# Kernel tuning notes

Hardware: AMD Instinct MI355X
Metric: run time of the kernel (lower is better)

Reference implementation:

```python
import jax, jax.numpy as jnp
import numpy as np

ATT_DIM = 1024
N_HEADS = 16
D_HEAD = ATT_DIM // N_HEADS
LARGE = 1e30  # fp32 masking constant used by masked_softmax


def setup_inputs() -> dict:
    key = jax.random.key(0)
    ks = jax.random.split(key, 12)
    B, Tq, Tv, D = 4, 2048, 2048, 1024
    s = 1.0 / np.sqrt(D)
    sf = 1.0 / np.sqrt(ATT_DIM)
    return {
        "query": jax.random.normal(ks[0], (B, Tq, D), jnp.float32),
        "value": jax.random.normal(ks[1], (B, Tv, D), jnp.float32),
        "value_lens": jax.random.randint(ks[2], (B,), 0, Tv, jnp.int32),
        "Wq": jax.random.normal(ks[3], (D, ATT_DIM), jnp.float32) * s,
        "bq": jnp.zeros((ATT_DIM,), jnp.float32),
        "Wk": jax.random.normal(ks[4], (D, ATT_DIM), jnp.float32) * s,
        "bk": jnp.zeros((ATT_DIM,), jnp.float32),
        "Wv": jax.random.normal(ks[5], (D, ATT_DIM), jnp.float32) * s,
        "bv": jnp.zeros((ATT_DIM,), jnp.float32),
        "Wf": jax.random.normal(ks[6], (ATT_DIM, ATT_DIM), jnp.float32) * sf,
        "bf": jnp.zeros((ATT_DIM,), jnp.float32),
    }


def _attention(query, value, value_lens, Wq, bq, Wk, bk, Wv, bv, Wf, bf):
    B, Tq, _ = query.shape
    Tv = value.shape[1]
    # projections
    k = value @ Wk + bk                     # [B,Tv,att_dim]
    v = value @ Wv + bv                     # [B,Tv,att_dim]
    q = (query @ Wq + bq) / jnp.sqrt(jnp.asarray(D_HEAD, query.dtype))
    # split heads
    q = q.reshape(B, Tq, N_HEADS, D_HEAD)
    k = k.reshape(B, Tv, N_HEADS, D_HEAD)
    v = v.reshape(B, Tv, N_HEADS, D_HEAD)
    # energy: [B, n_heads, Tq, Tv]
    energy = jnp.einsum("bind,bjnd->bnij", q, k)
    # sequence mask: [B,1,1,Tv]
    mask = (jnp.arange(Tv)[None, :] < value_lens[:, None]).astype(energy.dtype)
    energy = energy - (1.0 - mask)[:, None, None, :] * jnp.asarray(LARGE, energy.dtype)
    att_weight = jax.nn.softmax(energy, axis=-1)
    # context: [B, Tq, n_heads, d_head] -> [B, Tq, att_dim]
    context = jnp.einsum("bnij,bjnd->bind", att_weight, v).reshape(B, Tq, ATT_DIM)
    return context @ Wf + bf  # final_att (num_att_head > 1)


def reference(query, value, value_lens, Wq, bq, Wk, bk, Wv, bv, Wf, bf):
    return _attention(query, value, value_lens, Wq, bq, Wk, bk, Wv, bv, Wf, bf)
```

## Files before the change

### kernel.cpp

```cpp
#include <hip/hip_runtime.h>
#include <hip/hip_bf16.h>

typedef __attribute__((ext_vector_type(8))) short short8;
typedef __attribute__((ext_vector_type(4))) float f32x4;
typedef unsigned short u16;
typedef unsigned int u32;
typedef __attribute__((ext_vector_type(8))) unsigned short u16x8;
typedef __attribute__((ext_vector_type(4))) unsigned short u16x4;

__device__ __forceinline__ u16 f2bf(float f) {
    u32 u = __builtin_bit_cast(u32, f);
    u += 0x7FFFu + ((u >> 16) & 1u);
    return (u16)(u >> 16);
}
__device__ __forceinline__ u32 cvtpk(float a, float b) {
    u32 r;
    asm("v_cvt_pk_bf16_f32 %0, %1, %2" : "=v"(r) : "v"(a), "v"(b));
    return r;
}
__device__ __forceinline__ float fexp2(float x) {
    float r;
    asm("v_exp_f32 %0, %1" : "=v"(r) : "v"(x));
    return r;
}

__device__ __forceinline__ int swz(int row, int col) {
    return (row * 128 + col * 2) ^ ((row & 7) << 4);
}

__device__ __forceinline__ void gl16(const void* g, void* l) {
    __builtin_amdgcn_global_load_lds(
        (const __attribute__((address_space(1))) unsigned int*)g,
        (__attribute__((address_space(3))) unsigned int*)l, 16, 0, 0);
}

#define FENCE() asm volatile("" ::: "memory")
#define BARRIER() do { FENCE(); __builtin_amdgcn_s_barrier(); FENCE(); } while (0)

__global__ __launch_bounds__(256)
void prep_kernel(const float* __restrict__ query, const float* __restrict__ value,
                 u16* __restrict__ qB, u16* __restrict__ vB,
                 const float* __restrict__ W0, const float* __restrict__ W1,
                 const float* __restrict__ W2, const float* __restrict__ W3,
                 u16* __restrict__ T0, u16* __restrict__ T1,
                 u16* __restrict__ T2, u16* __restrict__ T3)
{
    int bid = blockIdx.x;
    if (bid < 8192) {
        const float* src; u16* dst;
        if (bid < 4096) { src = query; dst = qB; }
        else            { src = value; dst = vB; bid -= 4096; }
        const int i = bid * 256 + threadIdx.x;
        const float4 a = ((const float4*)src)[2 * i];
        const float4 b = ((const float4*)src)[2 * i + 1];
        u16x8 h;
        h[0] = f2bf(a.x); h[1] = f2bf(a.y); h[2] = f2bf(a.z); h[3] = f2bf(a.w);
        h[4] = f2bf(b.x); h[5] = f2bf(b.y); h[6] = f2bf(b.z); h[7] = f2bf(b.w);
        ((u16x8*)dst)[i] = h;
        return;
    }
    int b2 = bid - 8192;
    const int z = b2 >> 10; b2 &= 1023;
    const float* W; u16* T;
    switch (z) {
        case 0:  W = W0; T = T0; break;
        case 1:  W = W1; T = T1; break;
        case 2:  W = W2; T = T2; break;
        default: W = W3; T = T3; break;
    }
    __shared__ u16 tile[32][33];
    const int tid = threadIdx.x;
    const int n0 = (b2 & 31) * 32, k0 = (b2 >> 5) * 32;
    const int r = tid >> 3, c = (tid & 7) * 4;
    float4 v = *(const float4*)(W + (size_t)(k0 + r) * 1024 + n0 + c);
    tile[c + 0][r] = f2bf(v.x);
    tile[c + 1][r] = f2bf(v.y);
    tile[c + 2][r] = f2bf(v.z);
    tile[c + 3][r] = f2bf(v.w);
    __syncthreads();
    u16x4 h;
    h[0] = tile[r][c]; h[1] = tile[r][c + 1]; h[2] = tile[r][c + 2]; h[3] = tile[r][c + 3];
    *(u16x4*)(T + (size_t)(n0 + r) * 1024 + k0 + c) = h;
}

#define GNK 32

__device__ __forceinline__ void stage_a(const u16* __restrict__ A, unsigned char* bufA,
                                        int row0, int kt, int tid) {
    const int r = tid >> 2, s = tid & 3;
    gl16((const unsigned char*)A + (size_t)(row0 + r) * 2048 + kt * 64 + ((s ^ (r & 3)) << 4),
         bufA + tid * 16);
}
__device__ __forceinline__ void stage_b(const u16* __restrict__ BT, unsigned char* bufB,
                                        int col0, int kt, int hb, int tid) {
    const int r = hb * 128 + (tid >> 2), s = tid & 3;
    gl16((const unsigned char*)BT + (size_t)(col0 + r) * 2048 + kt * 64 + ((s ^ (r & 3)) << 4),
         bufB + hb * 8192 + tid * 16);
}

__device__ __forceinline__ void gemm_core(const u16* __restrict__ A, const u16* __restrict__ BT,
                                          int row0, int col0, unsigned char* smem,
                                          int tid, int wm, int wn, int l15, int lhi,
                                          f32x4 acc[4][4])
{
    const int slot = (lhi ^ (l15 & 3)) << 4;
    #pragma unroll
    for (int kt = 0; kt < 2; ++kt) {
        unsigned char* buf = smem + kt * 24576;
        stage_a(A, buf, row0, kt, tid);
        stage_b(BT, buf + 8192, col0, kt, 0, tid);
        stage_b(BT, buf + 8192, col0, kt, 1, tid);
    }
    asm volatile("s_waitcnt vmcnt(3)" ::: "memory");
    BARRIER();

    int cb = 0;
    for (int k = 0; k < GNK; ++k) {
        unsigned char* bufA = smem + cb * 24576;
        unsigned char* bufB = bufA + 8192;
        const bool st = (k + 2 < GNK);
        int nb = cb + 2; if (nb >= 3) nb -= 3;
        unsigned char* nbuf = smem + nb * 24576;
        cb = (cb == 2) ? 0 : cb + 1;

        short8 a0, a1, a2, a3, b0, b1;
        a0 = *(const short8*)(bufA + (wm * 64 + 0 * 16 + l15) * 64 + slot);
        a1 = *(const short8*)(bufA + (wm * 64 + 1 * 16 + l15) * 64 + slot);
        a2 = *(const short8*)(bufA + (wm * 64 + 2 * 16 + l15) * 64 + slot);
        a3 = *(const short8*)(bufA + (wm * 64 + 3 * 16 + l15) * 64 + slot);
        b0 = *(const short8*)(bufB + (wn * 64 + 0 * 16 + l15) * 64 + slot);
        b1 = *(const short8*)(bufB + (wn * 64 + 1 * 16 + l15) * 64 + slot);
        if (st) stage_a(A, nbuf, row0, k + 2, tid);
        BARRIER();
        __builtin_amdgcn_s_setprio(1);
        acc[0][0] = __builtin_amdgcn_mfma_f32_16x16x32_bf16(a0, b0, acc[0][0], 0, 0, 0);
        acc[0][1] = __builtin_amdgcn_mfma_f32_16x16x32_bf16(a0, b1, acc[0][1], 0, 0, 0);
        acc[1][0] = __builtin_amdgcn_mfma_f32_16x16x32_bf16(a1, b0, acc[1][0], 0, 0, 0);
        acc[1][1] = __builtin_amdgcn_mfma_f32_16x16x32_bf16(a1, b1, acc[1][1], 0, 0, 0);
        acc[2][0] = __builtin_amdgcn_mfma_f32_16x16x32_bf16(a2, b0, acc[2][0], 0, 0, 0);
        acc[2][1] = __builtin_amdgcn_mfma_f32_16x16x32_bf16(a2, b1, acc[2][1], 0, 0, 0);
        acc[3][0] = __builtin_amdgcn_mfma_f32_16x16x32_bf16(a3, b0, acc[3][0], 0, 0, 0);
        acc[3][1] = __builtin_amdgcn_mfma_f32_16x16x32_bf16(a3, b1, acc[3][1], 0, 0, 0);
        __builtin_amdgcn_s_setprio(0);
        BARRIER();

        short8 b2, b3;
        b2 = *(const short8*)(bufB + (wn * 64 + 2 * 16 + l15) * 64 + slot);
        b3 = *(const short8*)(bufB + (wn * 64 + 3 * 16 + l15) * 64 + slot);
        if (st) {
            stage_b(BT, nbuf + 8192, col0, k + 2, 0, tid);
            stage_b(BT, nbuf + 8192, col0, k + 2, 1, tid);
        }
        if (k < GNK - 2)       asm volatile("s_waitcnt vmcnt(3)" ::: "memory");
        else if (k == GNK - 2) asm volatile("s_waitcnt vmcnt(0)" ::: "memory");
        BARRIER();
        __builtin_amdgcn_s_setprio(1);
        acc[0][2] = __builtin_amdgcn_mfma_f32_16x16x32_bf16(a0, b2, acc[0][2], 0, 0, 0);
        acc[0][3] = __builtin_amdgcn_mfma_f32_16x16x32_bf16(a0, b3, acc[0][3], 0, 0, 0);
        acc[1][2] = __builtin_amdgcn_mfma_f32_16x16x32_bf16(a1, b2, acc[1][2], 0, 0, 0);
        acc[1][3] = __builtin_amdgcn_mfma_f32_16x16x32_bf16(a1, b3, acc[1][3], 0, 0, 0);
        acc[2][2] = __builtin_amdgcn_mfma_f32_16x16x32_bf16(a2, b2, acc[2][2], 0, 0, 0);
        acc[2][3] = __builtin_amdgcn_mfma_f32_16x16x32_bf16(a2, b3, acc[2][3], 0, 0, 0);
        acc[3][2] = __builtin_amdgcn_mfma_f32_16x16x32_bf16(a3, b2, acc[3][2], 0, 0, 0);
        acc[3][3] = __builtin_amdgcn_mfma_f32_16x16x32_bf16(a3, b3, acc[3][3], 0, 0, 0);
        __builtin_amdgcn_s_setprio(0);
        BARRIER();
    }
}

__global__ __launch_bounds__(512, 4)
void proj_kernel(const u16* __restrict__ queryB, const u16* __restrict__ valueB,
                 const u16* __restrict__ WqT, const u16* __restrict__ WkT,
                 const u16* __restrict__ WvT,
                 const float* __restrict__ bq, const float* __restrict__ bk,
                 const float* __restrict__ bv,
                 u16* __restrict__ Qb, u16* __restrict__ Kb, u16* __restrict__ Vt)
{
    __shared__ __align__(16) unsigned char smem[73728];
    const int t = (blockIdx.x & 7) * 96 + (blockIdx.x >> 3);
    const int z = t >> 8;
    const int tile = t & 255;
    const int row0 = (tile >> 2) * 128, col0 = (tile & 3) * 256;

    const u16* A    = (z == 0) ? queryB : valueB;
    const u16* BT   = (z == 0) ? WqT : (z == 1) ? WkT : WvT;
    const float* bias = (z == 0) ? bq : (z == 1) ? bk : bv;

    const int tid = threadIdx.x;
    const int lane = tid & 63, w = tid >> 6;
    const int wm = w >> 2, wn = w & 3;
    const int l15 = lane & 15, lhi = lane >> 4;

    f32x4 acc[4][4];
    const f32x4 fz = {0.f, 0.f, 0.f, 0.f};
    #pragma unroll
    for (int m = 0; m < 4; ++m)
        #pragma unroll
        for (int n = 0; n < 4; ++n) acc[m][n] = fz;

    gemm_core(A, BT, row0, col0, smem, tid, wm, wn, l15, lhi, acc);

    if (z < 2) {
        u16* out = (z == 0) ? Qb : Kb;
        const float scale = (z == 0) ? 0.18033688011112042f : 1.0f;
        const int bb = row0 >> 11;
        #pragma unroll
        for (int n = 0; n < 4; ++n) {
            int col = col0 + wn * 64 + n * 16 + l15;
            int hh = col >> 6, d = col & 63;
            float bv2 = bias[col];
            #pragma unroll
            for (int m = 0; m < 4; ++m) {
                int rbase = row0 + wm * 64 + m * 16 + lhi * 4;
                #pragma unroll
                for (int rr = 0; rr < 4; ++rr) {
                    int trow = (rbase + rr) & 2047;
                    out[(((size_t)bb * 16 + hh) * 2048 + trow) * 64 + d] =
                        f2bf((acc[m][n][rr] + bv2) * scale);
                }
            }
        }
    } else {
        __syncthreads();
        u16* vl = (u16*)smem;
        #pragma unroll
        for (int n = 0; n < 4; ++n) {
            int c = wn * 64 + n * 16 + l15;
            float bv2 = bias[col0 + c];
            #pragma unroll
            for (int m = 0; m < 4; ++m) {
                int rl = wm * 64 + m * 16 + lhi * 4;
                u16x4 h;
                #pragma unroll
                for (int rr = 0; rr < 4; ++rr) h[rr] = f2bf(acc[m][n][rr] + bv2);
                *(u16x4*)(vl + c * 132 + rl) = h;
            }
        }
        __syncthreads();
        const int bb = row0 >> 11, t0 = row0 & 2047;
        const int c = tid >> 1, hseg = tid & 1;
        const int col = col0 + c;
        const int hh = col >> 6, d = col & 63;
        size_t gb = (((size_t)bb * 16 + hh) * 64 + d) * 2048 + t0 + hseg * 64;
        #pragma unroll
        for (int j = 0; j < 8; ++j) {
            u16x8 v = *(const u16x8*)(vl + c * 132 + hseg * 64 + j * 8);
            *(u16x8*)(Vt + gb + j * 8) = v;
        }
    }
}

__global__ __launch_bounds__(512, 4)
void fgemm_kernel(const u16* __restrict__ Ctx, const u16* __restrict__ WfT,
                  const float* __restrict__ bias, float* __restrict__ out)
{
    __shared__ __align__(16) unsigned char smem[73728];
    const int t = (blockIdx.x & 7) * 32 + (blockIdx.x >> 3);
    const int row0 = (t >> 2) * 128, col0 = (t & 3) * 256;

    const int tid = threadIdx.x;
    const int lane = tid & 63, w = tid >> 6;
    const int wm = w >> 2, wn = w & 3;
    const int l15 = lane & 15, lhi = lane >> 4;

    f32x4 acc[4][4];
    const f32x4 fz = {0.f, 0.f, 0.f, 0.f};
    #pragma unroll
    for (int m = 0; m < 4; ++m)
        #pragma unroll
        for (int n = 0; n < 4; ++n) acc[m][n] = fz;

    gemm_core(Ctx, WfT, row0, col0, smem, tid, wm, wn, l15, lhi, acc);

    #pragma unroll
    for (int n = 0; n < 4; ++n) {
        int col = col0 + wn * 64 + n * 16 + l15;
        float bv2 = bias[col];
        #pragma unroll
        for (int m = 0; m < 4; ++m) {
            int rbase = row0 + wm * 64 + m * 16 + lhi * 4;
            #pragma unroll
            for (int rr = 0; rr < 4; ++rr)
                out[(size_t)(rbase + rr) * 1024 + col] = acc[m][n][rr] + bv2;
        }
    }
}

__global__ __launch_bounds__(512, 4)
void attn_kernel(const u16* __restrict__ Qb, const u16* __restrict__ Kb,
                 const u16* __restrict__ Vt, const int* __restrict__ lens,
                 u16* __restrict__ Ctx)
{
    __shared__ __align__(16) unsigned char ksm[2][8192];
    __shared__ __align__(16) unsigned char vsm[2][8192];

    const int tid = threadIdx.x;
    const int lane = tid & 63;
    const int w = tid >> 6;
    const int l15 = lane & 15, lhi = lane >> 4;
    const int u = blockIdx.x;
    const int b = (u >> 8) & 3;
    const int v = u & 255;
    const int qt = (v >> 3) & 15;
    const int hh = ((v >> 7) & 1) * 8 + (v & 7);
    const size_t head = (size_t)(b * 16 + hh);
    const unsigned char* Kbase = (const unsigned char*)Kb + head * (2048 * 128);
    const unsigned char* Vbase = (const unsigned char*)Vt + head * (2048 * 128);
    const unsigned char* Qbase = (const unsigned char*)Qb + head * (2048 * 128) + (size_t)qt * (128 * 128);

    const int o0 = w * 1024 + lane * 16;
    const int r0 = o0 >> 7;
    const int sc0 = (o0 & 127) ^ ((r0 & 7) << 4);

    const unsigned char* kp = Kbase + (size_t)r0 * 128 + sc0;
    const unsigned char* vp = Vbase + (size_t)r0 * 4096 + sc0;

    const int lens_b = lens[b];
    const bool uniform = (lens_b == 0);
    const int len = uniform ? 2048 : lens_b;
    const int nt = (len + 63) >> 6;
    const bool tail = (!uniform) && ((len & 63) != 0);

    auto stage = [&](int t, int bi) {
        gl16(kp + (size_t)t * 8192, ksm[bi] + o0);
        gl16(vp + (size_t)t * 128, vsm[bi] + o0);
    };
    stage(0, 0);

    short8 qa[2];
    #pragma unroll
    for (int ks = 0; ks < 2; ++ks)
        qa[ks] = *(const short8*)(Qbase + (w * 16 + l15) * 128 + ks * 64 + lhi * 16);

    short8 onesv;
    #pragma unroll
    for (int i = 0; i < 8; ++i) onesv[i] = (short)0x3F80;

    __syncthreads();

    float m = -1e30f;
    const f32x4 fz = {0.f, 0.f, 0.f, 0.f};
    f32x4 cs = fz;
    f32x4 cT[4];
    #pragma unroll
    for (int nf = 0; nf < 4; ++nf) cT[nf] = fz;

    const int srcA = l15 + (((2 * lhi) & 3) << 4);
    const int srcB = l15 + (((2 * lhi + 1) & 3) << 4);
    const bool hi = lhi >= 2;

    for (int t = 0; t < nt; ++t) {
        const int cur = t & 1;
        if (t + 1 < nt) stage(t + 1, cur ^ 1);

        f32x4 s[4];
        #pragma unroll
        for (int jf = 0; jf < 4; ++jf) s[jf] = fz;
        if (!uniform) {
            __builtin_amdgcn_s_setprio(1);
            #pragma unroll
            for (int ks = 0; ks < 2; ++ks)
                #pragma unroll
                for (int jf = 0; jf < 4; ++jf) {
                    short8 kb = *(const short8*)(ksm[cur] + swz(jf * 16 + l15, ks * 32 + lhi * 8));
                    s[jf] = __builtin_amdgcn_mfma_f32_16x16x32_bf16(kb, qa[ks], s[jf], 0, 0, 0);
                }
            __builtin_amdgcn_s_setprio(0);
            if (tail && t == nt - 1) {
                const int kvb = t * 64 + lhi * 4;
                #pragma unroll
                for (int jf = 0; jf < 4; ++jf)
                    #pragma unroll
                    for (int r = 0; r < 4; ++r)
                        if (kvb + jf * 16 + r >= len) s[jf][r] = -1e30f;
            }
        }
        f32x4 m4;
        #pragma unroll
        for (int r = 0; r < 4; ++r)
            m4[r] = fmaxf(fmaxf(s[0][r], s[1][r]), fmaxf(s[2][r], s[3][r]));
        float tmax = fmaxf(fmaxf(m4[0], m4[1]), fmaxf(m4[2], m4[3]));
        tmax = fmaxf(tmax, __shfl_xor(tmax, 16));
        tmax = fmaxf(tmax, __shfl_xor(tmax, 32));
        if (__any(tmax > m + 8.f)) {
            const float mnew = fmaxf(m, tmax);
            const float sc = fexp2(m - mnew);
            #pragma unroll
            for (int r = 0; r < 4; ++r) cs[r] *= sc;
            #pragma unroll
            for (int nf = 0; nf < 4; ++nf)
                #pragma unroll
                for (int r = 0; r < 4; ++r) cT[nf][r] *= sc;
            m = mnew;
        }
        #pragma unroll
        for (int jf = 0; jf < 4; ++jf)
            #pragma unroll
            for (int r = 0; r < 4; ++r)
                s[jf][r] = fexp2(s[jf][r] - m);
        u32 pk[4][2];
        #pragma unroll
        for (int jf = 0; jf < 4; ++jf) {
            pk[jf][0] = cvtpk(s[jf][0], s[jf][1]);
            pk[jf][1] = cvtpk(s[jf][2], s[jf][3]);
        }
        short8 pb[2];
        #pragma unroll
        for (int ks = 0; ks < 2; ++ks) {
            u32 a0, a1, a2, a3;
            { u32 x0 = (u32)__shfl((int)pk[2 * ks][0], srcA); u32 x1 = (u32)__shfl((int)pk[2 * ks + 1][0], srcA); a0 = hi ? x1 : x0; }
            { u32 x0 = (u32)__shfl((int)pk[2 * ks][1], srcA); u32 x1 = (u32)__shfl((int)pk[2 * ks + 1][1], srcA); a1 = hi ? x1 : x0; }
            { u32 x0 = (u32)__shfl((int)pk[2 * ks][0], srcB); u32 x1 = (u32)__shfl((int)pk[2 * ks + 1][0], srcB); a2 = hi ? x1 : x0; }
            { u32 x0 = (u32)__shfl((int)pk[2 * ks][1], srcB); u32 x1 = (u32)__shfl((int)pk[2 * ks + 1][1], srcB); a3 = hi ? x1 : x0; }
            typedef __attribute__((ext_vector_type(4))) unsigned int u32x4_t;
            u32x4_t av = {a0, a1, a2, a3};
            pb[ks] = __builtin_bit_cast(short8, av);
        }
        __builtin_amdgcn_s_setprio(1);
        #pragma unroll
        for (int ks = 0; ks < 2; ++ks) {
            cs = __builtin_amdgcn_mfma_f32_16x16x32_bf16(onesv, pb[ks], cs, 0, 0, 0);
            #pragma unroll
            for (int nf = 0; nf < 4; ++nf) {
                short8 vb = *(const short8*)(vsm[cur] + swz(nf * 16 + l15, ks * 32 + lhi * 8));
                cT[nf] = __builtin_amdgcn_mfma_f32_16x16x32_bf16(vb, pb[ks], cT[nf], 0, 0, 0);
            }
        }
        __builtin_amdgcn_s_setprio(0);
        __syncthreads();
    }

    const float inv = 1.0f / cs[0];
    const int trow = qt * 128 + w * 16 + l15;
    u16* op = Ctx + ((size_t)b * 2048 + trow) * 1024 + hh * 64 + lhi * 4;
    #pragma unroll
    for (int nf = 0; nf < 4; ++nf) {
        u16x4 h;
        #pragma unroll
        for (int r = 0; r < 4; ++r) h[r] = f2bf(cT[nf][r] * inv);
        *(u16x4*)(op + nf * 16) = h;
    }
}

extern "C" void kernel_launch(void* const* d_in, const int* in_sizes, int n_in,
                              void* d_out, int out_size, void* d_ws, size_t ws_size,
                              hipStream_t stream)
{
    (void)in_sizes; (void)n_in; (void)out_size; (void)ws_size;
    const float* query = (const float*)d_in[0];
    const float* value = (const float*)d_in[1];
    const int*   lens  = (const int*)d_in[2];
    const float* Wq = (const float*)d_in[3];
    const float* bq = (const float*)d_in[4];
    const float* Wk = (const float*)d_in[5];
    const float* bk = (const float*)d_in[6];
    const float* Wv = (const float*)d_in[7];
    const float* bv = (const float*)d_in[8];
    const float* Wf = (const float*)d_in[9];
    const float* bfp = (const float*)d_in[10];

    unsigned char* ws = (unsigned char*)d_ws;
    const size_t MB = (size_t)1 << 20;
    u16* WqT = (u16*)(ws + 0 * MB);
    u16* WkT = (u16*)(ws + 2 * MB);
    u16* WvT = (u16*)(ws + 4 * MB);
    u16* WfT = (u16*)(ws + 6 * MB);
    u16* Qb  = (u16*)(ws + 8 * MB);
    u16* Kb  = (u16*)(ws + 24 * MB);
    u16* Vt  = (u16*)(ws + 40 * MB);
    u16* Ctx = (u16*)(ws + 56 * MB);

    u16* queryB = (u16*)d_out;
    u16* valueB = queryB + (size_t)8192 * 1024;

    prep_kernel<<<dim3(12288), dim3(256), 0, stream>>>(query, value, queryB, valueB,
                                                       Wq, Wk, Wv, Wf, WqT, WkT, WvT, WfT);

    proj_kernel<<<dim3(768), dim3(512), 0, stream>>>(queryB, valueB, WqT, WkT, WvT,
                                                     bq, bk, bv, Qb, Kb, Vt);

    attn_kernel<<<dim3(1024), dim3(512), 0, stream>>>(Qb, Kb, Vt, lens, Ctx);

    fgemm_kernel<<<dim3(256), dim3(512), 0, stream>>>(Ctx, WfT, bfp, (float*)d_out);
}
```

Measured before the change: 173.9 us.

## Split KV range across two wave groups per block and loop batches inside block

Restructures the attention kernel so each 512-thread block handles 64 query rows for one head, with two groups of four waves each processing half of every 128-key tile. The two partial softmax states are merged through shared memory at the end. Each block now loops over all four batches, and the grid shrinks from 1024 to 512 blocks. The aim is better load balance across the variable value_lens and larger KV tiles per barrier, at the cost of 64KB of LDS (lower occupancy), an extra merge step, and serialised batch processing within a block.

Result: slower. 190.6 us (+9.7%).

```diff
diff --git a/kernel.cpp b/kernel.cpp
--- a/kernel.cpp
+++ b/kernel.cpp
@@ -26,6 +26,9 @@
 
 __device__ __forceinline__ int swz(int row, int col) {
     return (row * 128 + col * 2) ^ ((row & 7) << 4);
+}
+__device__ __forceinline__ int swzV(int row, int col) {
+    return (row * 256 + col * 2) ^ ((row & 7) << 4);
 }
 
 __device__ __forceinline__ void gl16(const void* g, void* l) {
@@ -291,154 +294,185 @@
                  const u16* __restrict__ Vt, const int* __restrict__ lens,
                  u16* __restrict__ Ctx)
 {
-    __shared__ __align__(16) unsigned char ksm[2][8192];
-    __shared__ __align__(16) unsigned char vsm[2][8192];
+    __shared__ __align__(16) unsigned char sm[65536];
+    float* mb1 = (float*)(sm + 16384);
+    float* mb2 = (float*)(sm + 49152);
 
     const int tid = threadIdx.x;
     const int lane = tid & 63;
     const int w = tid >> 6;
+    const int g = w >> 2;
+    const int wq = w & 3;
     const int l15 = lane & 15, lhi = lane >> 4;
+
     const int u = blockIdx.x;
-    const int b = (u >> 8) & 3;
-    const int v = u & 255;
-    const int qt = (v >> 3) & 15;
-    const int hh = ((v >> 7) & 1) * 8 + (v & 7);
-    const size_t head = (size_t)(b * 16 + hh);
-    const unsigned char* Kbase = (const unsigned char*)Kb + head * (2048 * 128);
-    const unsigned char* Vbase = (const unsigned char*)Vt + head * (2048 * 128);
-    const unsigned char* Qbase = (const unsigned char*)Qb + head * (2048 * 128) + (size_t)qt * (128 * 128);
-
-    const int o0 = w * 1024 + lane * 16;
-    const int r0 = o0 >> 7;
-    const int sc0 = (o0 & 127) ^ ((r0 & 7) << 4);
-
-    const unsigned char* kp = Kbase + (size_t)r0 * 128 + sc0;
-    const unsigned char* vp = Vbase + (size_t)r0 * 4096 + sc0;
-
-    const int lens_b = lens[b];
-    const bool uniform = (lens_b == 0);
-    const int len = uniform ? 2048 : lens_b;
-    const int nt = (len + 63) >> 6;
-    const bool tail = (!uniform) && ((len & 63) != 0);
-
-    auto stage = [&](int t, int bi) {
-        gl16(kp + (size_t)t * 8192, ksm[bi] + o0);
-        gl16(vp + (size_t)t * 128, vsm[bi] + o0);
-    };
-    stage(0, 0);
-
-    short8 qa[2];
-    #pragma unroll
-    for (int ks = 0; ks < 2; ++ks)
-        qa[ks] = *(const short8*)(Qbase + (w * 16 + l15) * 128 + ks * 64 + lhi * 16);
+    const int hh = ((u >> 3) & 1) * 8 + (u & 7);
+    const int qt = u >> 4;
+
+    const int o0 = tid * 16;
+    const int r0k = o0 >> 7;
+    const int sck = (o0 & 127) ^ ((r0k & 7) << 4);
+    const int r0v = o0 >> 8;
+    const int scv = (o0 & 255) ^ ((r0v & 7) << 4);
 
     short8 onesv;
     #pragma unroll
     for (int i = 0; i < 8; ++i) onesv[i] = (short)0x3F80;
 
-    __syncthreads();
-
-    float m = -1e30f;
-    const f32x4 fz = {0.f, 0.f, 0.f, 0.f};
-    f32x4 cs = fz;
-    f32x4 cT[4];
-    #pragma unroll
-    for (int nf = 0; nf < 4; ++nf) cT[nf] = fz;
-
     const int srcA = l15 + (((2 * lhi) & 3) << 4);
     const int srcB = l15 + (((2 * lhi + 1) & 3) << 4);
     const bool hi = lhi >= 2;
-
-    for (int t = 0; t < nt; ++t) {
-        const int cur = t & 1;
-        if (t + 1 < nt) stage(t + 1, cur ^ 1);
-
-        f32x4 s[4];
-        #pragma unroll
-        for (int jf = 0; jf < 4; ++jf) s[jf] = fz;
-        if (!uniform) {
+    const f32x4 fz = {0.f, 0.f, 0.f, 0.f};
+
+    for (int b = 0; b < 4; ++b) {
+        const size_t head = (size_t)(b * 16 + hh);
+        const unsigned char* Kp = (const unsigned char*)Kb + head * 262144 + r0k * 128 + sck;
+        const unsigned char* Vp = (const unsigned char*)Vt + head * 262144 + (size_t)r0v * 4096 + scv;
+        const unsigned char* Qbase = (const unsigned char*)Qb + head * 262144 + (size_t)qt * 8192;
+
+        const int lens_b = lens[b];
+        const bool uniform = (lens_b == 0);
+        const int len = uniform ? 2048 : lens_b;
+        const int nt = (len + 127) >> 7;
+        const bool tail = (!uniform) && ((len & 127) != 0);
+
+        auto stage = [&](int t, int bi) {
+            unsigned char* kd = sm + bi * 16384;
+            unsigned char* vd = sm + 32768 + bi * 16384;
+            gl16(Kp + (size_t)t * 16384,        kd + o0);
+            gl16(Kp + (size_t)t * 16384 + 8192, kd + o0 + 8192);
+            gl16(Vp + (size_t)t * 256,          vd + o0);
+            gl16(Vp + (size_t)t * 256 + 131072, vd + o0 + 8192);
+        };
+        stage(0, 0);
+
+        short8 qa[2];
+        #pragma unroll
+        for (int ks = 0; ks < 2; ++ks)
+            qa[ks] = *(const short8*)(Qbase + (wq * 16 + l15) * 128 + ks * 64 + lhi * 16);
+
+        float m = -1e30f;
+        f32x4 cs = fz;
+        f32x4 cT[4];
+        #pragma unroll
+        for (int nf = 0; nf < 4; ++nf) cT[nf] = fz;
+
+        __syncthreads();
+
+        for (int t = 0; t < nt; ++t) {
+            const int cur = t & 1;
+            if (t + 1 < nt) stage(t + 1, cur ^ 1);
+            const unsigned char* kcur = sm + cur * 16384;
+            const unsigned char* vcur = sm + 32768 + cur * 16384;
+
+            f32x4 s[4];
+            #pragma unroll
+            for (int jf = 0; jf < 4; ++jf) s[jf] = fz;
+            if (!uniform) {
+                __builtin_amdgcn_s_setprio(1);
+                #pragma unroll
+                for (int ks = 0; ks < 2; ++ks)
+                    #pragma unroll
+                    for (int jf = 0; jf < 4; ++jf) {
+                        short8 kb = *(const short8*)(kcur + swz(g * 64 + jf * 16 + l15, ks * 32 + lhi * 8));
+                        s[jf] = __builtin_amdgcn_mfma_f32_16x16x32_bf16(kb, qa[ks], s[jf], 0, 0, 0);
+                    }
+                __builtin_amdgcn_s_setprio(0);
+                if (tail && t == nt - 1) {
+                    const int kvb = t * 128 + g * 64 + lhi * 4;
+                    #pragma unroll
+                    for (int jf = 0; jf < 4; ++jf)
+                        #pragma unroll
+                        for (int r = 0; r < 4; ++r)
+                            if (kvb + jf * 16 + r >= len) s[jf][r] = -1e30f;
+                }
+            }
+            f32x4 m4;
+            #pragma unroll
+            for (int r = 0; r < 4; ++r)
+                m4[r] = fmaxf(fmaxf(s[0][r], s[1][r]), fmaxf(s[2][r], s[3][r]));
+            float tmax = fmaxf(fmaxf(m4[0], m4[1]), fmaxf(m4[2], m4[3]));
+            tmax = fmaxf(tmax, __shfl_xor(tmax, 16));
+            tmax = fmaxf(tmax, __shfl_xor(tmax, 32));
+            if (__any(tmax > m + 8.f)) {
+                const float mnew = fmaxf(m, tmax);
+                const float sc = fexp2(m - mnew);
+                #pragma unroll
+                for (int r = 0; r < 4; ++r) cs[r] *= sc;
+                #pragma unroll
+                for (int nf = 0; nf < 4; ++nf)
+                    #pragma unroll
+                    for (int r = 0; r < 4; ++r) cT[nf][r] *= sc;
+                m = mnew;
+            }
+            #pragma unroll
+            for (int jf = 0; jf < 4; ++jf)
+                #pragma unroll
+                for (int r = 0; r < 4; ++r)
+                    s[jf][r] = fexp2(s[jf][r] - m);
+            u32 pk[4][2];
+            #pragma unroll
+            for (int jf = 0; jf < 4; ++jf) {
+                pk[jf][0] = cvtpk(s[jf][0], s[jf][1]);
+                pk[jf][1] = cvtpk(s[jf][2], s[jf][3]);
+            }
+            short8 pb[2];
+            #pragma unroll
+            for (int ks = 0; ks < 2; ++ks) {
+                u32 a0, a1, a2, a3;
+                { u32 x0 = (u32)__shfl((int)pk[2 * ks][0], srcA); u32 x1 = (u32)__shfl((int)pk[2 * ks + 1][0], srcA); a0 = hi ? x1 : x0; }
+                { u32 x0 = (u32)__shfl((int)pk[2 * ks][1], srcA); u32 x1 = (u32)__shfl((int)pk[2 * ks + 1][1], srcA); a1 = hi ? x1 : x0; }
+                { u32 x0 = (u32)__shfl((int)pk[2 * ks][0], srcB); u32 x1 = (u32)__shfl((int)pk[2 * ks + 1][0], srcB); a2 = hi ? x1 : x0; }
+                { u32 x0 = (u32)__shfl((int)pk[2 * ks][1], srcB); u32 x1 = (u32)__shfl((int)pk[2 * ks + 1][1], srcB); a3 = hi ? x1 : x0; }
+                typedef __attribute__((ext_vector_type(4))) unsigned int u32x4_t;
+                u32x4_t av = {a0, a1, a2, a3};
+                pb[ks] = __builtin_bit_cast(short8, av);
+            }
             __builtin_amdgcn_s_setprio(1);
             #pragma unroll
-            for (int ks = 0; ks < 2; ++ks)
-                #pragma unroll
-                for (int jf = 0; jf < 4; ++jf) {
-                    short8 kb = *(const short8*)(ksm[cur] + swz(jf * 16 + l15, ks * 32 + lhi * 8));
-                    s[jf] = __builtin_amdgcn_mfma_f32_16x16x32_bf16(kb, qa[ks], s[jf], 0, 0, 0);
+            for (int ks = 0; ks < 2; ++ks) {
+                cs = __builtin_amdgcn_mfma_f32_16x16x32_bf16(onesv, pb[ks], cs, 0, 0, 0);
+                #pragma unroll
+                for (int nf = 0; nf < 4; ++nf) {
+                    short8 vb = *(const short8*)(vcur + swzV(nf * 16 + l15, g * 64 + ks * 32 + lhi * 8));
+                    cT[nf] = __builtin_amdgcn_mfma_f32_16x16x32_bf16(vb, pb[ks], cT[nf], 0, 0, 0);
                 }
+            }
             __builtin_amdgcn_s_setprio(0);
-            if (tail && t == nt - 1) {
-                const int kvb = t * 64 + lhi * 4;
-                #pragma unroll
-                for (int jf = 0; jf < 4; ++jf)
-                    #pragma unroll
-                    for (int r = 0; r < 4; ++r)
-                        if (kvb + jf * 16 + r >= len) s[jf][r] = -1e30f;
-            }
-        }
-        f32x4 m4;
-        #pragma unroll
-        for (int r = 0; r < 4; ++r)
-            m4[r] = fmaxf(fmaxf(s[0][r], s[1][r]), fmaxf(s[2][r], s[3][r]));
-        float tmax = fmaxf(fmaxf(m4[0], m4[1]), fmaxf(m4[2], m4[3]));
-        tmax = fmaxf(tmax, __shfl_xor(tmax, 16));
-        tmax = fmaxf(tmax, __shfl_xor(tmax, 32));
-        if (__any(tmax > m + 8.f)) {
-            const float mnew = fmaxf(m, tmax);
-            const float sc = fexp2(m - mnew);
-            #pragma unroll
-            for (int r = 0; r < 4; ++r) cs[r] *= sc;
-            #pragma unroll
-            for (int nf = 0; nf < 4; ++nf)
-                #pragma unroll
-                for (int r = 0; r < 4; ++r) cT[nf][r] *= sc;
-            m = mnew;
-        }
-        #pragma unroll
-        for (int jf = 0; jf < 4; ++jf)
-            #pragma unroll
-            for (int r = 0; r < 4; ++r)
-                s[jf][r] = fexp2(s[jf][r] - m);
-        u32 pk[4][2];
-        #pragma unroll
-        for (int jf = 0; jf < 4; ++jf) {
-            pk[jf][0] = cvtpk(s[jf][0], s[jf][1]);
-            pk[jf][1] = cvtpk(s[jf][2], s[jf][3]);
-        }
-        short8 pb[2];
-        #pragma unroll
-        for (int ks = 0; ks < 2; ++ks) {
-            u32 a0, a1, a2, a3;
-            { u32 x0 = (u32)__shfl((int)pk[2 * ks][0], srcA); u32 x1 = (u32)__shfl((int)pk[2 * ks + 1][0], srcA); a0 = hi ? x1 : x0; }
-            { u32 x0 = (u32)__shfl((int)pk[2 * ks][1], srcA); u32 x1 = (u32)__shfl((int)pk[2 * ks + 1][1], srcA); a1 = hi ? x1 : x0; }
-            { u32 x0 = (u32)__shfl((int)pk[2 * ks][0], srcB); u32 x1 = (u32)__shfl((int)pk[2 * ks + 1][0], srcB); a2 = hi ? x1 : x0; }
-            { u32 x0 = (u32)__shfl((int)pk[2 * ks][1], srcB); u32 x1 = (u32)__shfl((int)pk[2 * ks + 1][1], srcB); a3 = hi ? x1 : x0; }
-            typedef __attribute__((ext_vector_type(4))) unsigned int u32x4_t;
-            u32x4_t av = {a0, a1, a2, a3};
-            pb[ks] = __builtin_bit_cast(short8, av);
-        }
-        __builtin_amdgcn_s_setprio(1);
-        #pragma unroll
-        for (int ks = 0; ks < 2; ++ks) {
-            cs = __builtin_amdgcn_mfma_f32_16x16x32_bf16(onesv, pb[ks], cs, 0, 0, 0);
+            __syncthreads();
+        }
+
+        const int ix = (wq * 64 + lane) * 12;
+        if (g == 1) {
+            *(f32x4*)(mb1 + ix)     = cT[0];
+            *(f32x4*)(mb1 + ix + 4) = cT[1];
+            *(f32x4*)(mb2 + ix)     = cT[2];
+            *(f32x4*)(mb2 + ix + 4) = cT[3];
+            mb1[ix + 8] = m;
+            mb1[ix + 9] = cs[0];
+        }
+        __syncthreads();
+        if (g == 0) {
+            f32x4 cB[4];
+            cB[0] = *(const f32x4*)(mb1 + ix);
+            cB[1] = *(const f32x4*)(mb1 + ix + 4);
+            cB[2] = *(const f32x4*)(mb2 + ix);
+            cB[3] = *(const f32x4*)(mb2 + ix + 4);
+            const float mB = mb1[ix + 8], csB = mb1[ix + 9];
+            const float M  = fmaxf(m, mB);
+            const float sA = fexp2(m - M), sB = fexp2(mB - M);
+            const float inv = 1.0f / (cs[0] * sA + csB * sB);
+            const int trow = qt * 64 + wq * 16 + l15;
+            u16* op = Ctx + ((size_t)b * 2048 + trow) * 1024 + hh * 64 + lhi * 4;
             #pragma unroll
             for (int nf = 0; nf < 4; ++nf) {
-                short8 vb = *(const short8*)(vsm[cur] + swz(nf * 16 + l15, ks * 32 + lhi * 8));
-                cT[nf] = __builtin_amdgcn_mfma_f32_16x16x32_bf16(vb, pb[ks], cT[nf], 0, 0, 0);
-            }
-        }
-        __builtin_amdgcn_s_setprio(0);
-        __syncthreads();
-    }
-
-    const float inv = 1.0f / cs[0];
-    const int trow = qt * 128 + w * 16 + l15;
-    u16* op = Ctx + ((size_t)b * 2048 + trow) * 1024 + hh * 64 + lhi * 4;
-    #pragma unroll
-    for (int nf = 0; nf < 4; ++nf) {
-        u16x4 h;
-        #pragma unroll
-        for (int r = 0; r < 4; ++r) h[r] = f2bf(cT[nf][r] * inv);
-        *(u16x4*)(op + nf * 16) = h;
+                u16x4 h;
+                #pragma unroll
+                for (int r = 0; r < 4; ++r)
+                    h[r] = f2bf((cT[nf][r] * sA + cB[nf][r] * sB) * inv);
+                *(u16x4*)(op + nf * 16) = h;
+            }
+        }
     }
 }
 
@@ -479,7 +513,7 @@
     proj_kernel<<<dim3(768), dim3(512), 0, stream>>>(queryB, valueB, WqT, WkT, WvT,
                                                      bq, bk, bv, Qb, Kb, Vt);
 
-    attn_kernel<<<dim3(1024), dim3(512), 0, stream>>>(Qb, Kb, Vt, lens, Ctx);
+    attn_kernel<<<dim3(512), dim3(512), 0, stream>>>(Qb, Kb, Vt, lens, Ctx);
 
     fgemm_kernel<<<dim3(256), dim3(512), 0, stream>>>(Ctx, WfT, bfp, (float*)d_out);
 }
```
